# Kernel tuning notes

Hardware: AMD Instinct MI355X
Metric: run time of the kernel (lower is better)

## Reference

```python
import jax, jax.numpy as jnp
import numpy as np

NEG_BIG = -9.0e15  # matches torch's -9000000000000000.0 mask fill
ALPHA = 0.2        # leakyrelu negative slope


def setup_inputs() -> dict:
    key = jax.random.key(0)
    k1, k2, k3, k4, k5 = jax.random.split(key, 5)
    N, F_in, F_out = 4096, 512, 64
    stdv = 1.0 / np.sqrt(F_out)
    x = jax.random.normal(k1, (N, F_in), dtype=jnp.float32)
    adj = jax.random.randint(k2, (N, N), 0, 2, dtype=jnp.int32)
    W = jax.random.uniform(k3, (F_in, F_out), dtype=jnp.float32, minval=-stdv, maxval=stdv)
    a = jax.random.normal(k4, (2 * F_out, 1), dtype=jnp.float32) * 0.1
    bias = jax.random.uniform(k5, (F_out,), dtype=jnp.float32, minval=-stdv, maxval=stdv)
    return {"x": x, "adj": adj, "W": W, "a": a, "bias": bias}


def _gat_forward(x, adj, W, a, bias):
    N = x.shape[0]
    F_out = W.shape[1]
    h = x @ W  # (N, F)
    a1 = a[:F_out, 0]   # weights hitting the first concat half
    a2 = a[F_out:, 0]   # weights hitting the second concat half
    # First half: row k=i*N+j of the concat holds h_j  ->  e1[j] = h_j . a1
    e1 = h @ a1  # (N,)
    # Second half of this repo's concat is NOT h_i; exact index algebra:
    # second[k=i*N+j, r] = h[(r*N+i)//F, (((r*N+i)%F)*N + j) % F]
    # Since it depends on j only via j % F, build table T[i, t] (t = j % F).
    r = jnp.arange(F_out)[:, None]          # (F, 1)
    i = jnp.arange(N)[None, :]              # (1, N)
    m = r * N + i                           # (F, N)
    p = m // F_out                          # row index into h
    s0 = m % F_out
    t = jnp.arange(F_out)                   # (F,)
    col = (s0[..., None] * N + t) % F_out   # (F, N, F) column index into h
    vals = h[p[..., None], col]             # (F, N, F)
    T = jnp.einsum('r,rit->it', a2, vals)   # (N, F)
    j = jnp.arange(N)
    e2 = T[:, j % F_out]                    # (N, N) second-half contribution
    e = e1[None, :] + e2                    # (N, N) pre-activation scores
    e = jnp.where(e > 0, e, ALPHA * e)      # LeakyReLU(0.2)
    e = jnp.where(adj > 0, e, NEG_BIG)      # mask non-edges
    att = jax.nn.softmax(e, axis=1)         # row-wise softmax (dropout = eval identity)
    out = jax.nn.relu(att @ h) + bias       # relu BEFORE bias add, as in source
    return out


def reference(x, adj, W, a, bias):
    return _gat_forward(x, adj, W, a, bias)
```

## Files before the change

### kernel.cpp

```cpp
#include <hip/hip_runtime.h>
#include <math.h>

#define N_NODES 4096
#define F_IN    512
#define F_OUT   64
#define ALPHA   0.2f
#define NPART   8

typedef _Float16 half8 __attribute__((ext_vector_type(8)));
typedef _Float16 half4 __attribute__((ext_vector_type(4)));
typedef float    floatx4 __attribute__((ext_vector_type(4)));

union H8U4 { half8 h; uint32_t u[4]; };

__device__ __forceinline__ void async_copy16(void* lds, const void* g) {
    __builtin_amdgcn_global_load_lds(
        (const __attribute__((address_space(1))) unsigned int*)g,
        (__attribute__((address_space(3))) unsigned int*)lds, 16, 0, 0);
}

__global__ __launch_bounds__(256) void k_prep(const float* __restrict__ W,
                                              _Float16* __restrict__ WT) {
    int idx = blockIdx.x * 256 + threadIdx.x;
    int t = idx >> 9;
    int k = idx & 511;
    WT[idx] = (_Float16)W[k * F_OUT + t];
}

__global__ __launch_bounds__(512) void k_hW(const float* __restrict__ x,
                                            const _Float16* __restrict__ WT,
                                            const float* __restrict__ a,
                                            float* __restrict__ h,
                                            _Float16* __restrict__ hT,
                                            float* __restrict__ e1) {
    __shared__ float red[8][16][64];
    int tid  = threadIdx.x;
    int lane = tid & 63;
    int w    = tid >> 6;
    int i0   = blockIdx.x * 16;
    int n    = lane & 15;
    int quad = lane >> 4;

    floatx4 acc[4] = {{0,0,0,0},{0,0,0,0},{0,0,0,0},{0,0,0,0}};

    const float* xr = x + (size_t)(i0 + n) * F_IN + w * 64 + quad * 8;
    const _Float16* wb = WT + w * 64 + quad * 8;
#pragma unroll
    for (int kk = 0; kk < 64; kk += 32) {
        float4 x0 = *(const float4*)(xr + kk);
        float4 x1 = *(const float4*)(xr + kk + 4);
        half8 af = {(_Float16)x0.x, (_Float16)x0.y, (_Float16)x0.z, (_Float16)x0.w,
                    (_Float16)x1.x, (_Float16)x1.y, (_Float16)x1.z, (_Float16)x1.w};
#pragma unroll
        for (int g = 0; g < 4; ++g) {
            half8 bf = *(const half8*)(wb + (size_t)(g * 16 + n) * F_IN + kk);
            acc[g] = __builtin_amdgcn_mfma_f32_16x16x32_f16(af, bf, acc[g], 0, 0, 0);
        }
    }
#pragma unroll
    for (int g = 0; g < 4; ++g)
#pragma unroll
        for (int r = 0; r < 4; ++r)
            red[w][g * 4 + r][lane] = acc[g][r];
    __syncthreads();
    if (w != 0) return;
#pragma unroll
    for (int g = 0; g < 4; ++g)
#pragma unroll
        for (int r = 0; r < 4; ++r) {
            float v = 0.f;
#pragma unroll
            for (int ww = 0; ww < 8; ++ww)
                v += red[ww][g * 4 + r][lane];
            acc[g][r] = v;
        }
#pragma unroll
    for (int g = 0; g < 4; ++g) {
        half4 hv;
#pragma unroll
        for (int r = 0; r < 4; ++r) {
            h[(size_t)(i0 + quad * 4 + r) * F_OUT + g * 16 + n] = acc[g][r];
            hv[r] = (_Float16)acc[g][r];
        }
        *(half4*)(hT + (size_t)(g * 16 + n) * N_NODES + i0 + quad * 4) = hv;
    }
    float a1v[4];
#pragma unroll
    for (int g = 0; g < 4; ++g) a1v[g] = a[g * 16 + n];
#pragma unroll
    for (int r = 0; r < 4; ++r) {
        float v = acc[0][r] * a1v[0] + acc[1][r] * a1v[1] + acc[2][r] * a1v[2] + acc[3][r] * a1v[3];
        v += __shfl_xor(v, 1, 64);
        v += __shfl_xor(v, 2, 64);
        v += __shfl_xor(v, 4, 64);
        v += __shfl_xor(v, 8, 64);
        if (n == 0) e1[i0 + quad * 4 + r] = v;
    }
}

__global__ __launch_bounds__(256, 3) void k_main(const int* __restrict__ adj,
                                                 const float* __restrict__ h,
                                                 const float* __restrict__ e1,
                                                 const float* __restrict__ a,
                                                 const _Float16* __restrict__ hT,
                                                 float* __restrict__ out_part,
                                                 float* __restrict__ den_part) {
    __shared__ int      lds_adj[4][8][256];
    __shared__ _Float16 lds_B[16][512];
    __shared__ _Float16 lds_P[512];
    __shared__ float    lds_part[4][64];
    __shared__ float    TqS[64];

    int tid  = threadIdx.x;
    int lane = tid & 63;
    int w    = tid >> 6;
    int b    = blockIdx.x;
    int rb   = b >> 3;
    int s    = b & 7;
    int i0   = rb * 64 + w * 16;
    int n    = lane & 15;
    int quad = lane >> 4;

    {
        int t  = tid & 63;
        int rp = tid >> 6;
        const float* a2 = a + F_OUT;
        float ssum = 0.f;
#pragma unroll
        for (int rr = 0; rr < 16; ++rr) {
            int r = rp * 16 + rr;
            ssum += a2[r] * h[(size_t)r * 4096 + rb * 64 + t];
        }
        lds_part[rp][t] = ssum;
    }
    __syncthreads();
    if (tid < 64)
        TqS[tid] = lds_part[0][tid] + lds_part[1][tid] + lds_part[2][tid] + lds_part[3][tid];
    __syncthreads();
    {
        int j = s * 512 + tid * 2;
        float2 ev = *(const float2*)(e1 + j);
        float e0 = ev.x + TqS[(tid * 2) & 63];
        float e1v = ev.y + TqS[(tid * 2 + 1) & 63];
        e0  = e0  > 0.f ? e0  : ALPHA * e0;
        e1v = e1v > 0.f ? e1v : ALPHA * e1v;
        lds_P[tid * 2]     = (_Float16)__expf(e0);
        lds_P[tid * 2 + 1] = (_Float16)__expf(e1v);
    }

    floatx4 acc[4] = {{0,0,0,0},{0,0,0,0},{0,0,0,0},{0,0,0,0}};
    floatx4 accd = {0, 0, 0, 0};
    _Float16 one_h = (n == 0) ? (_Float16)1.0f : (_Float16)0.0f;
    half8 ones_f = {one_h, one_h, one_h, one_h, one_h, one_h, one_h, one_h};

    for (int it = 0; it < 4; ++it) {
        int jb = s * 512 + it * 128;
        const int* adj_base = adj + (size_t)(i0 + n) * N_NODES + jb + quad * 8;
#pragma unroll
        for (int c = 0; c < 4; ++c) {
            async_copy16(&lds_adj[w][c * 2 + 0][0], adj_base + c * 32);
            async_copy16(&lds_adj[w][c * 2 + 1][0], adj_base + c * 32 + 4);
        }
        const _Float16* hT_base = hT + (size_t)(w * 16 + n) * N_NODES + jb + quad * 8;
#pragma unroll
        for (int c = 0; c < 4; ++c)
            async_copy16(&lds_B[w * 4 + c][0], hT_base + c * 32);
        __syncthreads();

#pragma unroll
        for (int c = 0; c < 4; ++c) {
            int4 ga = *(const int4*)&lds_adj[w][c * 2 + 0][lane * 4];
            int4 gb = *(const int4*)&lds_adj[w][c * 2 + 1][lane * 4];
            H8U4 pv, af;
            pv.h = *(const half8*)&lds_P[it * 128 + c * 32 + quad * 8];
            af.u[0] = pv.u[0] & ((ga.x > 0 ? 0x0000FFFFu : 0u) | (ga.y > 0 ? 0xFFFF0000u : 0u));
            af.u[1] = pv.u[1] & ((ga.z > 0 ? 0x0000FFFFu : 0u) | (ga.w > 0 ? 0xFFFF0000u : 0u));
            af.u[2] = pv.u[2] & ((gb.x > 0 ? 0x0000FFFFu : 0u) | (gb.y > 0 ? 0xFFFF0000u : 0u));
            af.u[3] = pv.u[3] & ((gb.z > 0 ? 0x0000FFFFu : 0u) | (gb.w > 0 ? 0xFFFF0000u : 0u));
#pragma unroll
            for (int g4 = 0; g4 < 4; ++g4) {
                half8 bf = *(const half8*)&lds_B[g4 * 4 + c][lane * 8];
                acc[g4] = __builtin_amdgcn_mfma_f32_16x16x32_f16(af.h, bf, acc[g4], 0, 0, 0);
            }
            accd = __builtin_amdgcn_mfma_f32_16x16x32_f16(af.h, ones_f, accd, 0, 0, 0);
        }
        __syncthreads();
    }

    float* op = out_part + ((size_t)s * N_NODES + i0) * F_OUT;
#pragma unroll
    for (int g4 = 0; g4 < 4; ++g4)
#pragma unroll
        for (int r = 0; r < 4; ++r)
            op[(quad * 4 + r) * F_OUT + g4 * 16 + n] = acc[g4][r];
    if (n == 0) {
#pragma unroll
        for (int r = 0; r < 4; ++r)
            den_part[s * N_NODES + i0 + quad * 4 + r] = accd[r];
    }
}

__global__ __launch_bounds__(128) void k_out(const float* __restrict__ out_part,
                                             const float* __restrict__ den_part,
                                             const float* __restrict__ bias,
                                             float* __restrict__ out) {
    int idx4 = blockIdx.x * 128 + threadIdx.x;
    int base = idx4 * 4;
    int i = base >> 6;
    int t = base & 63;
    float4 sacc = {0.f, 0.f, 0.f, 0.f};
    float dacc = 0.f;
#pragma unroll
    for (int p = 0; p < NPART; ++p) {
        float4 v = ((const float4*)(out_part + (size_t)p * N_NODES * F_OUT))[idx4];
        sacc.x += v.x; sacc.y += v.y; sacc.z += v.z; sacc.w += v.w;
        dacc += den_part[p * N_NODES + i];
    }
    float4 bv = *(const float4*)(bias + t);
    float4 o;
    o.x = fmaxf(sacc.x / dacc, 0.f) + bv.x;
    o.y = fmaxf(sacc.y / dacc, 0.f) + bv.y;
    o.z = fmaxf(sacc.z / dacc, 0.f) + bv.z;
    o.w = fmaxf(sacc.w / dacc, 0.f) + bv.w;
    ((float4*)out)[idx4] = o;
}

extern "C" void kernel_launch(void* const* d_in, const int* in_sizes, int n_in,
                              void* d_out, int out_size, void* d_ws, size_t ws_size,
                              hipStream_t stream) {
    const float* x    = (const float*)d_in[0];
    const int*   adj  = (const int*)d_in[1];
    const float* W    = (const float*)d_in[2];
    const float* a    = (const float*)d_in[3];
    const float* bias = (const float*)d_in[4];
    float* out = (float*)d_out;

    char* ws = (char*)d_ws;
    float*    h        = (float*)ws;
    _Float16* hT       = (_Float16*)(ws + 1024 * 1024);
    float*    e1       = (float*)(ws + 1536 * 1024);
    _Float16* WT       = (_Float16*)(ws + 1552 * 1024);
    float*    out_part = (float*)(ws + 2128 * 1024);
    float*    den_part = (float*)(ws + (2128 + 8192) * 1024);

    k_prep<<<128, 256, 0, stream>>>(W, WT);
    k_hW  <<<256, 512, 0, stream>>>(x, WT, a, h, hT, e1);
    k_main<<<512, 256, 0, stream>>>(adj, h, e1, a, hT, out_part, den_part);
    k_out <<<512, 128, 0, stream>>>(out_part, den_part, bias, out);
}
```

Before: 120.5 us.

## Fuse W transpose into hW and partial reduction into main via last-block atomics

Measured after the change: 190.3 us. +57.9%, slower.

```diff
diff --git a/kernel.cpp b/kernel.cpp
--- a/kernel.cpp
+++ b/kernel.cpp
@@ -19,20 +19,13 @@
         (__attribute__((address_space(3))) unsigned int*)lds, 16, 0, 0);
 }
 
-__global__ __launch_bounds__(256) void k_prep(const float* __restrict__ W,
-                                              _Float16* __restrict__ WT) {
-    int idx = blockIdx.x * 256 + threadIdx.x;
-    int t = idx >> 9;
-    int k = idx & 511;
-    WT[idx] = (_Float16)W[k * F_OUT + t];
-}
-
 __global__ __launch_bounds__(512) void k_hW(const float* __restrict__ x,
-                                            const _Float16* __restrict__ WT,
+                                            const float* __restrict__ W,
                                             const float* __restrict__ a,
                                             float* __restrict__ h,
                                             _Float16* __restrict__ hT,
-                                            float* __restrict__ e1) {
+                                            float* __restrict__ e1,
+                                            int* __restrict__ flags) {
     __shared__ float red[8][16][64];
     int tid  = threadIdx.x;
     int lane = tid & 63;
@@ -41,19 +34,23 @@
     int n    = lane & 15;
     int quad = lane >> 4;
 
+    if (blockIdx.x == 0 && tid < 64) flags[tid] = 0;
+
     floatx4 acc[4] = {{0,0,0,0},{0,0,0,0},{0,0,0,0},{0,0,0,0}};
 
     const float* xr = x + (size_t)(i0 + n) * F_IN + w * 64 + quad * 8;
-    const _Float16* wb = WT + w * 64 + quad * 8;
 #pragma unroll
     for (int kk = 0; kk < 64; kk += 32) {
         float4 x0 = *(const float4*)(xr + kk);
         float4 x1 = *(const float4*)(xr + kk + 4);
         half8 af = {(_Float16)x0.x, (_Float16)x0.y, (_Float16)x0.z, (_Float16)x0.w,
                     (_Float16)x1.x, (_Float16)x1.y, (_Float16)x1.z, (_Float16)x1.w};
+        int k0 = w * 64 + kk + quad * 8;
 #pragma unroll
         for (int g = 0; g < 4; ++g) {
-            half8 bf = *(const half8*)(wb + (size_t)(g * 16 + n) * F_IN + kk);
+            const float* wc = W + (size_t)k0 * F_OUT + g * 16 + n;
+            half8 bf = {(_Float16)wc[0 * 64], (_Float16)wc[1 * 64], (_Float16)wc[2 * 64], (_Float16)wc[3 * 64],
+                        (_Float16)wc[4 * 64], (_Float16)wc[5 * 64], (_Float16)wc[6 * 64], (_Float16)wc[7 * 64]};
             acc[g] = __builtin_amdgcn_mfma_f32_16x16x32_f16(af, bf, acc[g], 0, 0, 0);
         }
     }
@@ -104,12 +101,16 @@
                                                  const float* __restrict__ a,
                                                  const _Float16* __restrict__ hT,
                                                  float* __restrict__ out_part,
-                                                 float* __restrict__ den_part) {
+                                                 float* __restrict__ den_part,
+                                                 int* __restrict__ flags,
+                                                 const float* __restrict__ bias,
+                                                 float* __restrict__ out) {
     __shared__ int      lds_adj[4][8][256];
     __shared__ _Float16 lds_B[16][512];
     __shared__ _Float16 lds_P[512];
     __shared__ float    lds_part[4][64];
     __shared__ float    TqS[64];
+    __shared__ int      is_last;
 
     int tid  = threadIdx.x;
     int lane = tid & 63;
@@ -198,31 +199,35 @@
         for (int r = 0; r < 4; ++r)
             den_part[s * N_NODES + i0 + quad * 4 + r] = accd[r];
     }
-}
-
-__global__ __launch_bounds__(128) void k_out(const float* __restrict__ out_part,
-                                             const float* __restrict__ den_part,
-                                             const float* __restrict__ bias,
-                                             float* __restrict__ out) {
-    int idx4 = blockIdx.x * 128 + threadIdx.x;
-    int base = idx4 * 4;
-    int i = base >> 6;
-    int t = base & 63;
-    float4 sacc = {0.f, 0.f, 0.f, 0.f};
-    float dacc = 0.f;
-#pragma unroll
-    for (int p = 0; p < NPART; ++p) {
-        float4 v = ((const float4*)(out_part + (size_t)p * N_NODES * F_OUT))[idx4];
-        sacc.x += v.x; sacc.y += v.y; sacc.z += v.z; sacc.w += v.w;
-        dacc += den_part[p * N_NODES + i];
-    }
-    float4 bv = *(const float4*)(bias + t);
-    float4 o;
-    o.x = fmaxf(sacc.x / dacc, 0.f) + bv.x;
-    o.y = fmaxf(sacc.y / dacc, 0.f) + bv.y;
-    o.z = fmaxf(sacc.z / dacc, 0.f) + bv.z;
-    o.w = fmaxf(sacc.w / dacc, 0.f) + bv.w;
-    ((float4*)out)[idx4] = o;
+
+    __threadfence();
+    if (tid == 0)
+        is_last = (atomicAdd(&flags[rb], 1) == NPART - 1);
+    __syncthreads();
+    if (!is_last) return;
+    __threadfence();
+
+    int i0g = rb * 64;
+#pragma unroll
+    for (int e = tid; e < 1024; e += 256) {
+        int row = e >> 4;
+        int c4  = e & 15;
+        float4 sacc = {0.f, 0.f, 0.f, 0.f};
+        float dacc = 0.f;
+#pragma unroll
+        for (int p = 0; p < NPART; ++p) {
+            float4 v = *(const float4*)(out_part + ((size_t)p * N_NODES + i0g + row) * F_OUT + c4 * 4);
+            sacc.x += v.x; sacc.y += v.y; sacc.z += v.z; sacc.w += v.w;
+            dacc += den_part[p * N_NODES + i0g + row];
+        }
+        float4 bv = *(const float4*)(bias + c4 * 4);
+        float4 o;
+        o.x = fmaxf(sacc.x / dacc, 0.f) + bv.x;
+        o.y = fmaxf(sacc.y / dacc, 0.f) + bv.y;
+        o.z = fmaxf(sacc.z / dacc, 0.f) + bv.z;
+        o.w = fmaxf(sacc.w / dacc, 0.f) + bv.w;
+        *(float4*)(out + (size_t)(i0g + row) * F_OUT + c4 * 4) = o;
+    }
 }
 
 extern "C" void kernel_launch(void* const* d_in, const int* in_sizes, int n_in,
@@ -239,12 +244,10 @@
     float*    h        = (float*)ws;
     _Float16* hT       = (_Float16*)(ws + 1024 * 1024);
     float*    e1       = (float*)(ws + 1536 * 1024);
-    _Float16* WT       = (_Float16*)(ws + 1552 * 1024);
-    float*    out_part = (float*)(ws + 2128 * 1024);
-    float*    den_part = (float*)(ws + (2128 + 8192) * 1024);
-
-    k_prep<<<128, 256, 0, stream>>>(W, WT);
-    k_hW  <<<256, 512, 0, stream>>>(x, WT, a, h, hT, e1);
-    k_main<<<512, 256, 0, stream>>>(adj, h, e1, a, hT, out_part, den_part);
-    k_out <<<512, 128, 0, stream>>>(out_part, den_part, bias, out);
-}
+    float*    out_part = (float*)(ws + 2048 * 1024);
+    float*    den_part = (float*)(ws + (2048 + 8192) * 1024);
+    int*      flags    = (int*)(ws + (2048 + 8192 + 128) * 1024);
+
+    k_hW  <<<256, 512, 0, stream>>>(x, W, a, h, hT, e1, flags);
+    k_main<<<512, 256, 0, stream>>>(adj, h, e1, a, hT, out_part, den_part, flags, bias, out);
+}
```

## Pack adjacency into a bitmask in the prep kernel and read bits in main

Applied to the files above, without the earlier changes.

New measurement: 122.0 us. About the same (+1.2%).

```diff
diff --git a/kernel.cpp b/kernel.cpp
--- a/kernel.cpp
+++ b/kernel.cpp
@@ -19,12 +19,30 @@
         (__attribute__((address_space(3))) unsigned int*)lds, 16, 0, 0);
 }
 
-__global__ __launch_bounds__(256) void k_prep(const float* __restrict__ W,
-                                              _Float16* __restrict__ WT) {
-    int idx = blockIdx.x * 256 + threadIdx.x;
-    int t = idx >> 9;
-    int k = idx & 511;
-    WT[idx] = (_Float16)W[k * F_OUT + t];
+__global__ __launch_bounds__(256) void k_prep2(const float* __restrict__ W,
+                                               _Float16* __restrict__ WT,
+                                               const int* __restrict__ adj,
+                                               uint32_t* __restrict__ bm) {
+    int gb = blockIdx.x;
+    if (gb < 2048) {
+        int wid = gb * 256 + threadIdx.x;
+        const int* p = adj + (size_t)wid * 32;
+        uint32_t m = 0;
+#pragma unroll
+        for (int q = 0; q < 8; ++q) {
+            int4 v = *(const int4*)(p + q * 4);
+            m |= (v.x > 0 ? 1u : 0u) << (q * 4 + 0);
+            m |= (v.y > 0 ? 1u : 0u) << (q * 4 + 1);
+            m |= (v.z > 0 ? 1u : 0u) << (q * 4 + 2);
+            m |= (v.w > 0 ? 1u : 0u) << (q * 4 + 3);
+        }
+        bm[wid] = m;
+    } else {
+        int idx = (gb - 2048) * 256 + threadIdx.x;
+        int t = idx >> 9;
+        int k = idx & 511;
+        WT[idx] = (_Float16)W[k * F_OUT + t];
+    }
 }
 
 __global__ __launch_bounds__(512) void k_hW(const float* __restrict__ x,
@@ -98,14 +116,13 @@
     }
 }
 
-__global__ __launch_bounds__(256, 3) void k_main(const int* __restrict__ adj,
+__global__ __launch_bounds__(256, 3) void k_main(const uint32_t* __restrict__ bm,
                                                  const float* __restrict__ h,
                                                  const float* __restrict__ e1,
                                                  const float* __restrict__ a,
                                                  const _Float16* __restrict__ hT,
                                                  float* __restrict__ out_part,
                                                  float* __restrict__ den_part) {
-    __shared__ int      lds_adj[4][8][256];
     __shared__ _Float16 lds_B[16][512];
     __shared__ _Float16 lds_P[512];
     __shared__ float    lds_part[4][64];
@@ -120,6 +137,14 @@
     int i0   = rb * 64 + w * 16;
     int n    = lane & 15;
     int quad = lane >> 4;
+
+    const uint32_t* bmr = bm + (size_t)(i0 + n) * (N_NODES / 32) + s * 16;
+    uint4 bwa = *(const uint4*)(bmr + 0);
+    uint4 bwb = *(const uint4*)(bmr + 4);
+    uint4 bwc = *(const uint4*)(bmr + 8);
+    uint4 bwd = *(const uint4*)(bmr + 12);
+    uint32_t bw[16] = {bwa.x, bwa.y, bwa.z, bwa.w, bwb.x, bwb.y, bwb.z, bwb.w,
+                       bwc.x, bwc.y, bwc.z, bwc.w, bwd.x, bwd.y, bwd.z, bwd.w};
 
     {
         int t  = tid & 63;
@@ -153,14 +178,9 @@
     _Float16 one_h = (n == 0) ? (_Float16)1.0f : (_Float16)0.0f;
     half8 ones_f = {one_h, one_h, one_h, one_h, one_h, one_h, one_h, one_h};
 
+#pragma unroll
     for (int it = 0; it < 4; ++it) {
         int jb = s * 512 + it * 128;
-        const int* adj_base = adj + (size_t)(i0 + n) * N_NODES + jb + quad * 8;
-#pragma unroll
-        for (int c = 0; c < 4; ++c) {
-            async_copy16(&lds_adj[w][c * 2 + 0][0], adj_base + c * 32);
-            async_copy16(&lds_adj[w][c * 2 + 1][0], adj_base + c * 32 + 4);
-        }
         const _Float16* hT_base = hT + (size_t)(w * 16 + n) * N_NODES + jb + quad * 8;
 #pragma unroll
         for (int c = 0; c < 4; ++c)
@@ -169,14 +189,13 @@
 
 #pragma unroll
         for (int c = 0; c < 4; ++c) {
-            int4 ga = *(const int4*)&lds_adj[w][c * 2 + 0][lane * 4];
-            int4 gb = *(const int4*)&lds_adj[w][c * 2 + 1][lane * 4];
+            uint32_t mbyte = bw[it * 4 + c] >> (quad * 8);
             H8U4 pv, af;
             pv.h = *(const half8*)&lds_P[it * 128 + c * 32 + quad * 8];
-            af.u[0] = pv.u[0] & ((ga.x > 0 ? 0x0000FFFFu : 0u) | (ga.y > 0 ? 0xFFFF0000u : 0u));
-            af.u[1] = pv.u[1] & ((ga.z > 0 ? 0x0000FFFFu : 0u) | (ga.w > 0 ? 0xFFFF0000u : 0u));
-            af.u[2] = pv.u[2] & ((gb.x > 0 ? 0x0000FFFFu : 0u) | (gb.y > 0 ? 0xFFFF0000u : 0u));
-            af.u[3] = pv.u[3] & ((gb.z > 0 ? 0x0000FFFFu : 0u) | (gb.w > 0 ? 0xFFFF0000u : 0u));
+            af.u[0] = pv.u[0] & (((mbyte &   1u) ? 0x0000FFFFu : 0u) | ((mbyte &   2u) ? 0xFFFF0000u : 0u));
+            af.u[1] = pv.u[1] & (((mbyte &   4u) ? 0x0000FFFFu : 0u) | ((mbyte &   8u) ? 0xFFFF0000u : 0u));
+            af.u[2] = pv.u[2] & (((mbyte &  16u) ? 0x0000FFFFu : 0u) | ((mbyte &  32u) ? 0xFFFF0000u : 0u));
+            af.u[3] = pv.u[3] & (((mbyte &  64u) ? 0x0000FFFFu : 0u) | ((mbyte & 128u) ? 0xFFFF0000u : 0u));
 #pragma unroll
             for (int g4 = 0; g4 < 4; ++g4) {
                 half8 bf = *(const half8*)&lds_B[g4 * 4 + c][lane * 8];
@@ -240,11 +259,12 @@
     _Float16* hT       = (_Float16*)(ws + 1024 * 1024);
     float*    e1       = (float*)(ws + 1536 * 1024);
     _Float16* WT       = (_Float16*)(ws + 1552 * 1024);
-    float*    out_part = (float*)(ws + 2128 * 1024);
-    float*    den_part = (float*)(ws + (2128 + 8192) * 1024);
-
-    k_prep<<<128, 256, 0, stream>>>(W, WT);
-    k_hW  <<<256, 512, 0, stream>>>(x, WT, a, h, hT, e1);
-    k_main<<<512, 256, 0, stream>>>(adj, h, e1, a, hT, out_part, den_part);
-    k_out <<<512, 128, 0, stream>>>(out_part, den_part, bias, out);
-}
+    uint32_t* bm       = (uint32_t*)(ws + 2128 * 1024);
+    float*    out_part = (float*)(ws + 4176 * 1024);
+    float*    den_part = (float*)(ws + (4176 + 8192) * 1024);
+
+    k_prep2<<<2176, 256, 0, stream>>>(W, WT, adj, bm);
+    k_hW   <<<256, 512, 0, stream>>>(x, WT, a, h, hT, e1);
+    k_main <<<512, 256, 0, stream>>>(bm, h, e1, a, hT, out_part, den_part);
+    k_out  <<<512, 128, 0, stream>>>(out_part, den_part, bias, out);
+}
```
